# Performance work log

Hardware: AMD Instinct MI355X
Metric: run time of the kernel (lower is better)

## Reference

```python
import jax, jax.numpy as jnp
import numpy as np

D_MODEL = 512
N_HEADS = 8
D_HEAD = D_MODEL // N_HEADS
SCALE = D_HEAD ** -0.5


def _rel_shift(x):
    # x: (b, h, qlen, klen) -> Transformer-XL relative shift
    b, h, qlen, klen = x.shape
    x = jnp.pad(x, ((0, 0), (0, 0), (0, 0), (1, 0)))        # (b,h,q,k+1)
    x = x.reshape(b, h, klen + 1, qlen)
    x = x[:, :, 1:, :].reshape(b, h, qlen, klen)
    return x


def setup_inputs() -> dict:
    key = jax.random.key(0)
    ks = jax.random.split(key, 12)
    B, S = 2, 2048
    P = 2 * S - 1
    w = lambda k, shape: (jax.random.normal(k, shape, jnp.float32) * 0.02)
    return {
        "x": jax.random.normal(ks[0], (B, S, D_MODEL), jnp.float32),
        "pos_emb": jax.random.normal(ks[1], (P, D_MODEL), jnp.float32),
        "Wq": w(ks[2], (D_MODEL, D_MODEL)), "bq": jnp.zeros((D_MODEL,), jnp.float32),
        "Wk": w(ks[3], (D_MODEL, D_MODEL)), "bk": jnp.zeros((D_MODEL,), jnp.float32),
        "Wv": w(ks[4], (D_MODEL, D_MODEL)), "bv": jnp.zeros((D_MODEL,), jnp.float32),
        "Wp": w(ks[5], (D_MODEL, D_MODEL)),
        "Wo": w(ks[6], (D_MODEL, D_MODEL)), "bo": jnp.zeros((D_MODEL,), jnp.float32),
        "pos_bias_u": w(ks[7], (N_HEADS, D_HEAD)),
        "pos_bias_v": w(ks[8], (N_HEADS, D_HEAD)),
    }


def reference(x, pos_emb, Wq, bq, Wk, bk, Wv, bv, Wp, Wo, bo, pos_bias_u, pos_bias_v):
    B, S, _ = x.shape
    # projections (torch Linear: y = x @ W^T + b; here W stored as (in, out))
    q = (x @ Wq + bq).reshape(B, S, N_HEADS, D_HEAD)
    k = (x @ Wk + bk).reshape(B, S, N_HEADS, D_HEAD)
    v = (x @ Wv + bv).reshape(B, S, N_HEADS, D_HEAD)
    p = (pos_emb @ Wp).reshape(-1, N_HEADS, D_HEAD)  # (2S-1, H, D)

    # content score: (q + u) @ k^T  -> (B,H,S,S)
    content = jnp.einsum("bshd,bthd->bhst", q + pos_bias_u, k)
    # position score: (q + v_bias) @ p^T -> (B,H,S,2S-1), then rel_shift
    pos = jnp.einsum("bshd,phd->bhsp", q + pos_bias_v, p)
    pos = _rel_shift(pos)[..., :S]  # trim to kv_len

    attn = jax.nn.softmax((content + pos) * SCALE, axis=-1)
    out = jnp.einsum("bhst,bthd->bshd", attn, v).reshape(B, S, D_MODEL)
    out = out @ Wo + bo
    return out
```

## Files before the change

kernel.cpp:

```cpp
#include <hip/hip_runtime.h>

#define DM    512
#define NH    8
#define DH    64
#define SEQ   2048
#define PLEN  4095
#define NB    2
#define ATT_SCALE 0.125f

typedef __attribute__((ext_vector_type(8))) _Float16 half8;
typedef __attribute__((ext_vector_type(4))) float   floatx4;

__device__ __forceinline__ void gll16(const _Float16* g, _Float16* l) {
    __builtin_amdgcn_global_load_lds(
        (const __attribute__((address_space(1))) void*)g,
        (__attribute__((address_space(3))) void*)l, 16, 0, 0);
}

__global__ __launch_bounds__(256)
void prep(const float* __restrict__ x, const float* __restrict__ pe,
          const float* __restrict__ W0, const float* __restrict__ W1,
          const float* __restrict__ W2, const float* __restrict__ W3,
          const float* __restrict__ W4,
          _Float16* __restrict__ x16, _Float16* __restrict__ pe16,
          _Float16* __restrict__ Wt)
{
    __shared__ _Float16 tile[64 * 72];
    const int z = blockIdx.z;
    const int t = threadIdx.x;

    if (z < 2) {
        const float* src = z ? pe : x;
        _Float16* dst = z ? pe16 : x16;
        const long n = z ? (long)PLEN * DM : (long)NB * SEQ * DM;
        const long i = ((long)blockIdx.x * 256 + t) * 8;
        if (i >= n) return;
        float4 f0 = *(const float4*)(src + i);
        float4 f1 = *(const float4*)(src + i + 4);
        half8 o;
        o[0] = (_Float16)f0.x; o[1] = (_Float16)f0.y;
        o[2] = (_Float16)f0.z; o[3] = (_Float16)f0.w;
        o[4] = (_Float16)f1.x; o[5] = (_Float16)f1.y;
        o[6] = (_Float16)f1.z; o[7] = (_Float16)f1.w;
        *(half8*)(dst + i) = o;
        return;
    }
    if (blockIdx.x >= 64) return;
    const int wz = z - 2;
    const float* W = (wz == 0) ? W0 : (wz == 1) ? W1 : (wz == 2) ? W2
                   : (wz == 3) ? W3 : W4;
    _Float16* dst_base = Wt + (size_t)wz * DM * DM;
    const int n0 = (blockIdx.x & 7) * 64, k0 = (blockIdx.x >> 3) * 64;
    {
        const int kr = t >> 2, nch = (t & 3) * 16;
        const float* src = W + (size_t)(k0 + kr) * DM + n0 + nch;
        float4 f0 = *(const float4*)(src + 0);
        float4 f1 = *(const float4*)(src + 4);
        float4 f2 = *(const float4*)(src + 8);
        float4 f3 = *(const float4*)(src + 12);
        _Float16* trow = &tile[kr * 72 + nch];
        trow[0]  = (_Float16)f0.x; trow[1]  = (_Float16)f0.y;
        trow[2]  = (_Float16)f0.z; trow[3]  = (_Float16)f0.w;
        trow[4]  = (_Float16)f1.x; trow[5]  = (_Float16)f1.y;
        trow[6]  = (_Float16)f1.z; trow[7]  = (_Float16)f1.w;
        trow[8]  = (_Float16)f2.x; trow[9]  = (_Float16)f2.y;
        trow[10] = (_Float16)f2.z; trow[11] = (_Float16)f2.w;
        trow[12] = (_Float16)f3.x; trow[13] = (_Float16)f3.y;
        trow[14] = (_Float16)f3.z; trow[15] = (_Float16)f3.w;
    }
    __syncthreads();
    {
        const int nr = t >> 2, kch = (t & 3) * 16;
        half8 o0, o1;
#pragma unroll
        for (int i = 0; i < 8; ++i) o0[i] = tile[(kch + i) * 72 + nr];
#pragma unroll
        for (int i = 0; i < 8; ++i) o1[i] = tile[(kch + 8 + i) * 72 + nr];
        _Float16* dst = dst_base + (size_t)(n0 + nr) * DM + k0 + kch;
        *(half8*)dst = o0;
        *(half8*)(dst + 8) = o1;
    }
}

__global__ __launch_bounds__(256)
void gemm_qkvp(const _Float16* __restrict__ X, const _Float16* __restrict__ Pe,
               const _Float16* __restrict__ Wt,
               const float* __restrict__ bq, const float* __restrict__ bk,
               const float* __restrict__ bv, const float* __restrict__ bu,
               const float* __restrict__ bvb,
               _Float16* __restrict__ qu16, _Float16* __restrict__ qv16,
               _Float16* __restrict__ k16, _Float16* __restrict__ vt16,
               _Float16* __restrict__ p16)
{
    __shared__ _Float16 smem[32768];

    const int t = threadIdx.x;
    const int w = t >> 6, lane = t & 63, quad = lane >> 4, l16 = lane & 15;
    const int wr = w >> 1, wc = w & 1;
    const int l3 = lane >> 3, pos = lane & 7;
    const int z = blockIdx.z;
    const int n0 = blockIdx.x * 128;
    const int m0 = blockIdx.y * 128;

    const _Float16* A = (z == 3) ? Pe : X;
    const _Float16* Wz = Wt + (size_t)z * DM * DM;

    const int kx = l16 & 7;
    const int hox0 = ((quad) ^ kx) * 8;
    const int hox1 = ((4 + quad) ^ kx) * 8;

    floatx4 acc[4][4];
#pragma unroll
    for (int i = 0; i < 4; ++i)
#pragma unroll
        for (int j = 0; j < 4; ++j) acc[i][j] = (floatx4){0.f, 0.f, 0.f, 0.f};

#define QSTAGE(CUR, K0)                                                        \
    { _Float16* aB = smem + (CUR) * 16384;                                     \
      _Float16* wB = aB + 8192;                                                \
      _Pragma("unroll") for (int I = 0; I < 4; ++I) {                          \
        const int gr = I * 32 + w * 8 + l3;                                    \
        const int ch = pos ^ l3;                                               \
        int ar = m0 + gr; if (z == 3 && ar > PLEN - 1) ar = PLEN - 1;          \
        gll16(A + (size_t)ar * DM + (K0) + ch * 8, aB + I * 2048 + w * 512);   \
        gll16(Wz + (size_t)(n0 + gr) * DM + (K0) + ch * 8,                     \
              wB + I * 2048 + w * 512); } }

    QSTAGE(0, 0);
    int cur = 0;
    for (int k0 = 0; k0 < DM; k0 += 64) {
        asm volatile("s_waitcnt vmcnt(0)" ::: "memory");
        __builtin_amdgcn_s_barrier();
        asm volatile("" ::: "memory");
        if (k0 + 64 < DM) QSTAGE(cur ^ 1, k0 + 64);
        const _Float16* aB = smem + cur * 16384;
        const _Float16* wB = aB + 8192;
#pragma unroll
        for (int kb = 0; kb < 2; ++kb) {
            const int hox = kb ? hox1 : hox0;
            half8 af[4], bf[4];
#pragma unroll
            for (int i = 0; i < 4; ++i)
                af[i] = *(const half8*)&aB[(wr * 64 + i * 16 + l16) * 64 + hox];
#pragma unroll
            for (int j = 0; j < 4; ++j)
                bf[j] = *(const half8*)&wB[(wc * 64 + j * 16 + l16) * 64 + hox];
#pragma unroll
            for (int i = 0; i < 4; ++i)
#pragma unroll
                for (int j = 0; j < 4; ++j)
                    acc[i][j] = __builtin_amdgcn_mfma_f32_16x16x32_f16(
                        af[i], bf[j], acc[i][j], 0, 0, 0);
        }
        cur ^= 1;
    }
#undef QSTAGE

    const int hh = (n0 >> 6) + wc;
    const int bb = m0 >> 11;
    const int sbase = (m0 & 2047) + wr * 64;

    if (z == 0) {
#pragma unroll
        for (int j = 0; j < 4; ++j) {
            const int n = n0 + wc * 64 + j * 16 + l16;
            const int d = j * 16 + l16 - (wc ? 64 : 0) + (wc ? 64 : 0);
            const float bval = bq[n], uval = bu[n], vval = bvb[n];
#pragma unroll
            for (int i = 0; i < 4; ++i)
#pragma unroll
                for (int r = 0; r < 4; ++r) {
                    const int s = sbase + i * 16 + 4 * quad + r;
                    const size_t dst = ((size_t)((hh * NB + bb) * SEQ) + s) * DH + (n & 63);
                    const float q = acc[i][j][r] + bval;
                    qu16[dst] = (_Float16)((q + uval) * ATT_SCALE);
                    qv16[dst] = (_Float16)((q + vval) * ATT_SCALE);
                }
            (void)d;
        }
    } else if (z == 1) {
#pragma unroll
        for (int j = 0; j < 4; ++j) {
            const int n = n0 + wc * 64 + j * 16 + l16;
            const float bval = bk[n];
#pragma unroll
            for (int i = 0; i < 4; ++i)
#pragma unroll
                for (int r = 0; r < 4; ++r) {
                    const int s = sbase + i * 16 + 4 * quad + r;
                    k16[((size_t)((hh * NB + bb) * SEQ) + s) * DH + (n & 63)] =
                        (_Float16)(acc[i][j][r] + bval);
                }
        }
    } else if (z == 2) {
        __syncthreads();
        _Float16* tr = smem;
#pragma unroll
        for (int j = 0; j < 4; ++j) {
            const int ncol = wc * 64 + j * 16 + l16;
            const float bval = bv[n0 + ncol];
#pragma unroll
            for (int i = 0; i < 4; ++i)
#pragma unroll
                for (int r = 0; r < 4; ++r)
                    tr[(wr * 64 + i * 16 + 4 * quad + r) * 132 + ncol] =
                        (_Float16)(acc[i][j][r] + bval);
        }
        __syncthreads();
        {
            const int col = t >> 1;
            const int half = t & 1;
            const int h2 = (n0 + col) >> 6, d = (n0 + col) & 63;
            const int s0 = (m0 & 2047) + half * 64;
            _Float16* dst = vt16 + ((size_t)((h2 * NB + bb) * DH) + d) * SEQ + s0;
#pragma unroll
            for (int c = 0; c < 8; ++c) {
                half8 o;
#pragma unroll
                for (int k = 0; k < 8; ++k)
                    o[k] = tr[(half * 64 + c * 8 + k) * 132 + col];
                *(half8*)(dst + c * 8) = o;
            }
        }
    } else {
#pragma unroll
        for (int j = 0; j < 4; ++j) {
            const int n = n0 + wc * 64 + j * 16 + l16;
#pragma unroll
            for (int i = 0; i < 4; ++i)
#pragma unroll
                for (int r = 0; r < 4; ++r) {
                    const int m = m0 + wr * 64 + i * 16 + 4 * quad + r;
                    if (m < PLEN)
                        p16[((size_t)hh * PLEN + m) * DH + (n & 63)] =
                            (_Float16)acc[i][j][r];
                }
        }
    }
}

__global__ __launch_bounds__(256, 3)
void relattn_mfma(const _Float16* __restrict__ QU,
                  const _Float16* __restrict__ QV,
                  const _Float16* __restrict__ Kp,
                  const _Float16* __restrict__ VT,
                  const _Float16* __restrict__ Pp,
                  float* __restrict__ Opart,
                  float* __restrict__ Lpart)
{
    __shared__ _Float16 kbuf[2 * 4096];
    __shared__ _Float16 vbuf[4096];
    __shared__ _Float16 pring[2 * 4096];
    __shared__ _Float16 tS[64 * 72];

    const int t = threadIdx.x;
    const int w = t >> 6, lane = t & 63, quad = lane >> 4, l16 = lane & 15;
    const int i0 = blockIdx.x * 64;
    const int h = blockIdx.y;
    const int b = blockIdx.z & 1, jh = blockIdx.z >> 1;
    const size_t hb = (size_t)(h * NB + b);
    const int cbase = 48 - 16 * w;
    const int jbeg = jh * (SEQ / 2), jend = jbeg + (SEQ / 2);

    half8 qa[2], va[2];
    {
        const _Float16* qrow = QU + (hb * SEQ + i0 + 16 * w + l16) * DH + quad * 8;
        const _Float16* vrow = QV + (hb * SEQ + i0 + 16 * w + l16) * DH + quad * 8;
        qa[0] = *(const half8*)qrow;       qa[1] = *(const half8*)(qrow + 32);
        va[0] = *(const half8*)vrow;       va[1] = *(const half8*)(vrow + 32);
    }

    floatx4 O[4];
    float lsum[4] = {0.f, 0.f, 0.f, 0.f};
#pragma unroll
    for (int ct = 0; ct < 4; ++ct) O[ct] = (floatx4){0.f, 0.f, 0.f, 0.f};

    const _Float16* Kbase = Kp + hb * SEQ * DH;
    const _Float16* Vbase = VT + hb * DH * SEQ;
    const _Float16* Pbase = Pp + (size_t)h * PLEN * DH;
    const int rbase0 = (SEQ - 1) - i0 - 63;
    const int w0beg  = rbase0 + jbeg;

    const int kx = l16 & 7;
    const int hox0 = ((quad) ^ kx) * 8;
    const int hox1 = ((4 + quad) ^ kx) * 8;

    const int l3 = lane >> 3, pos = lane & 7;

    int prow64[5], pcar[5];
#pragma unroll
    for (int c2 = 0; c2 < 5; ++c2) {
        const int off = cbase + 16 * c2 + l16;
        prow64[c2] = (off & 63) * 64;
        pcar[c2]   = (off >> 6) & 1;
    }

#define STAGE_K(DST, J0)                                                       \
    { _Pragma("unroll") for (int I = 0; I < 2; ++I) {                          \
        const int cid = w * 2 + I;                                             \
        const int row = cid * 8 + l3;                                          \
        gll16(Kbase + (size_t)((J0) + row) * DH + ((pos ^ l3) << 3),           \
              (DST) + cid * 512); } }

#define STAGE_V(J0)                                                            \
    { _Pragma("unroll") for (int I = 0; I < 2; ++I) {                          \
        const int cid = w * 2 + I;                                             \
        const int row = cid * 8 + l3;                                          \
        gll16(Vbase + (size_t)row * SEQ + (J0) + ((pos ^ l3) << 3),            \
              vbuf + cid * 512); } }

#define STAGE_P(RELB)                                                         \
    { _Float16* pdst = pring + ((((RELB) >> 6) & 1) * 4096);                  \
      _Pragma("unroll") for (int I = 0; I < 2; ++I) {                         \
        const int cid = w * 2 + I;                                            \
        int ar = w0beg + (RELB) + cid * 8 + l3;                               \
        if (ar > PLEN - 1) ar = PLEN - 1;                                     \
        gll16(Pbase + (size_t)ar * DH + ((pos ^ l3) << 3),                    \
              pdst + cid * 512); } }

    STAGE_K(kbuf, jbeg);
    STAGE_P(0);
    STAGE_P(64);

    int cur = 0, par = 0;
    for (int j0 = jbeg; j0 < jend; j0 += 64) {
        asm volatile("s_waitcnt vmcnt(0)" ::: "memory");
        __builtin_amdgcn_s_barrier();
        asm volatile("" ::: "memory");

        const _Float16* kS = kbuf + cur * 4096;
        const bool more = (j0 + 64 < jend);

        STAGE_V(j0);
        if (more) STAGE_K(kbuf + (cur ^ 1) * 4096, j0 + 64);

        floatx4 Tacc[5];
#pragma unroll
        for (int c2 = 0; c2 < 5; ++c2) Tacc[c2] = (floatx4){0.f, 0.f, 0.f, 0.f};
#pragma unroll
        for (int c2 = 0; c2 < 5; ++c2) {
            const _Float16* pp = pring + ((pcar[c2] ^ par) * 4096) + prow64[c2];
            half8 bf0 = *(const half8*)(pp + hox0);
            half8 bf1 = *(const half8*)(pp + hox1);
            Tacc[c2] = __builtin_amdgcn_mfma_f32_16x16x32_f16(va[0], bf0, Tacc[c2], 0, 0, 0);
            Tacc[c2] = __builtin_amdgcn_mfma_f32_16x16x32_f16(va[1], bf1, Tacc[c2], 0, 0, 0);
        }

        asm volatile("" ::: "memory");
        __builtin_amdgcn_s_barrier();
        asm volatile("" ::: "memory");
        if (more) STAGE_P((j0 - jbeg) + 128);

        floatx4 Sc[4];
#pragma unroll
        for (int ct = 0; ct < 4; ++ct) Sc[ct] = (floatx4){0.f, 0.f, 0.f, 0.f};
#pragma unroll
        for (int ct = 0; ct < 4; ++ct) {
            half8 bf0 = *(const half8*)&kS[(16 * ct + l16) * 64 + hox0];
            half8 bf1 = *(const half8*)&kS[(16 * ct + l16) * 64 + hox1];
            Sc[ct] = __builtin_amdgcn_mfma_f32_16x16x32_f16(qa[0], bf0, Sc[ct], 0, 0, 0);
            Sc[ct] = __builtin_amdgcn_mfma_f32_16x16x32_f16(qa[1], bf1, Sc[ct], 0, 0, 0);
        }

#pragma unroll
        for (int r = 0; r < 4; ++r) {
            const int u  = l16 - 4 * quad - r + 15;
            const int dl = u & 15;
            const int s  = u >> 4;
            const int pidx = (((quad << 4) | dl) << 2);
            float rot[5];
#pragma unroll
            for (int c2 = 0; c2 < 5; ++c2)
                rot[c2] = __int_as_float(__builtin_amdgcn_ds_bpermute(
                    pidx, __float_as_int(Tacc[c2][r])));
#pragma unroll
            for (int ct = 0; ct < 4; ++ct) {
                const float tv = s ? rot[ct + 1] : rot[ct];
                const float e = __expf(Sc[ct][r] + tv);
                Sc[ct][r] = e;
                lsum[r] += e;
            }
        }

#pragma unroll
        for (int ct = 0; ct < 4; ++ct)
#pragma unroll
            for (int r = 0; r < 4; ++r)
                tS[(16 * w + 4 * quad + r) * 72 + 16 * ct + l16] = (_Float16)Sc[ct][r];
        asm volatile("" ::: "memory");

        if (more) asm volatile("s_waitcnt vmcnt(4)" ::: "memory");
        else      asm volatile("s_waitcnt vmcnt(0)" ::: "memory");
        __builtin_amdgcn_s_barrier();
        asm volatile("" ::: "memory");

#pragma unroll
        for (int kb = 0; kb < 2; ++kb) {
            half8 af = *(const half8*)&tS[(16 * w + l16) * 72 + kb * 32 + quad * 8];
            const int hox = kb ? hox1 : hox0;
#pragma unroll
            for (int ct = 0; ct < 4; ++ct) {
                half8 bf = *(const half8*)&vbuf[(16 * ct + l16) * 64 + hox];
                O[ct] = __builtin_amdgcn_mfma_f32_16x16x32_f16(af, bf, O[ct], 0, 0, 0);
            }
        }
        asm volatile("" ::: "memory");
        cur ^= 1; par ^= 1;
    }
#undef STAGE_K
#undef STAGE_V
#undef STAGE_P

    float* Op = Opart + (size_t)jh * NB * SEQ * DM;
    float* Lp = Lpart + (size_t)jh * NH * NB * SEQ;
#pragma unroll
    for (int r = 0; r < 4; ++r) {
#pragma unroll
        for (int m = 1; m < 16; m <<= 1) lsum[r] += __shfl_xor(lsum[r], m);
        const int row = i0 + 16 * w + 4 * quad + r;
        if (l16 == 0) Lp[hb * SEQ + row] = lsum[r];
        float* orow = Op + (size_t)(b * SEQ + row) * DM + h * DH;
#pragma unroll
        for (int ct = 0; ct < 4; ++ct)
            orow[16 * ct + l16] = O[ct][r];
    }
}

__global__ __launch_bounds__(256)
void attn_combine(const float* __restrict__ O0, const float* __restrict__ O1,
                  const float* __restrict__ L0, const float* __restrict__ L1,
                  _Float16* __restrict__ Out)
{
    const int e = (blockIdx.x * 256 + threadIdx.x) * 8;
    const int m = e >> 9;
    const int col = e & 511;
    const int h = col >> 6;
    const int b = m >> 11, i = m & 2047;
    const int li = (h * NB + b) * SEQ + i;
    const float inv = 1.f / (L0[li] + L1[li]);
    float4 a0 = *(const float4*)(O0 + e);
    float4 a1 = *(const float4*)(O0 + e + 4);
    float4 c0 = *(const float4*)(O1 + e);
    float4 c1 = *(const float4*)(O1 + e + 4);
    half8 o;
    o[0] = (_Float16)((a0.x + c0.x) * inv);
    o[1] = (_Float16)((a0.y + c0.y) * inv);
    o[2] = (_Float16)((a0.z + c0.z) * inv);
    o[3] = (_Float16)((a0.w + c0.w) * inv);
    o[4] = (_Float16)((a1.x + c1.x) * inv);
    o[5] = (_Float16)((a1.y + c1.y) * inv);
    o[6] = (_Float16)((a1.z + c1.z) * inv);
    o[7] = (_Float16)((a1.w + c1.w) * inv);
    *(half8*)(Out + e) = o;
}

__global__ __launch_bounds__(256)
void gemm_out(const _Float16* __restrict__ A, const _Float16* __restrict__ Wt,
              const float* __restrict__ bias, float* __restrict__ Out)
{
    __shared__ _Float16 aS[64 * 72];
    __shared__ _Float16 wS[64 * 72];

    const int t = threadIdx.x;
    const int w = t >> 6, lane = t & 63, quad = lane >> 4, l16 = lane & 15;
    const int n0 = blockIdx.x * 64;
    const int m0 = blockIdx.y * 64;
    const int srow = t >> 2, sch = (t & 3) * 16;

    const _Float16* arowp = A + (size_t)(m0 + srow) * DM + sch;
    const _Float16* wrowp = Wt + (size_t)(n0 + srow) * DM + sch;

    floatx4 acc[4];
#pragma unroll
    for (int ct = 0; ct < 4; ++ct) acc[ct] = (floatx4){0.f, 0.f, 0.f, 0.f};

    half8 pa0 = *(const half8*)arowp;
    half8 pa1 = *(const half8*)(arowp + 8);
    half8 pw0 = *(const half8*)wrowp;
    half8 pw1 = *(const half8*)(wrowp + 8);

    for (int k0 = 0; k0 < DM; k0 += 64) {
        __syncthreads();
        *(half8*)&aS[srow * 72 + sch]     = pa0;
        *(half8*)&aS[srow * 72 + sch + 8] = pa1;
        *(half8*)&wS[srow * 72 + sch]     = pw0;
        *(half8*)&wS[srow * 72 + sch + 8] = pw1;
        __syncthreads();
        if (k0 + 64 < DM) {
            pa0 = *(const half8*)(arowp + k0 + 64);
            pa1 = *(const half8*)(arowp + k0 + 72);
            pw0 = *(const half8*)(wrowp + k0 + 64);
            pw1 = *(const half8*)(wrowp + k0 + 72);
        }
#pragma unroll
        for (int kb = 0; kb < 2; ++kb) {
            half8 af = *(const half8*)&aS[(16 * w + l16) * 72 + kb * 32 + quad * 8];
#pragma unroll
            for (int ct = 0; ct < 4; ++ct) {
                half8 bf = *(const half8*)&wS[(16 * ct + l16) * 72 + kb * 32 + quad * 8];
                acc[ct] = __builtin_amdgcn_mfma_f32_16x16x32_f16(af, bf, acc[ct], 0, 0, 0);
            }
        }
    }

#pragma unroll
    for (int ct = 0; ct < 4; ++ct) {
        const int n = n0 + 16 * ct + l16;
        const float bval = bias[n];
#pragma unroll
        for (int r = 0; r < 4; ++r) {
            const int m = m0 + 16 * w + 4 * quad + r;
            Out[(size_t)m * DM + n] = acc[ct][r] + bval;
        }
    }
}

extern "C" void kernel_launch(void* const* d_in, const int* in_sizes, int n_in,
                              void* d_out, int out_size, void* d_ws, size_t ws_size,
                              hipStream_t stream)
{
    (void)in_sizes; (void)n_in; (void)out_size; (void)ws_size;
    const float* x   = (const float*)d_in[0];
    const float* pe  = (const float*)d_in[1];
    const float* Wq  = (const float*)d_in[2];
    const float* bq  = (const float*)d_in[3];
    const float* Wk  = (const float*)d_in[4];
    const float* bk  = (const float*)d_in[5];
    const float* Wv  = (const float*)d_in[6];
    const float* bv  = (const float*)d_in[7];
    const float* Wp  = (const float*)d_in[8];
    const float* Wo  = (const float*)d_in[9];
    const float* bo  = (const float*)d_in[10];
    const float* pbu = (const float*)d_in[11];
    const float* pbv = (const float*)d_in[12];
    float* out = (float*)d_out;

    const size_t nX  = (size_t)NB * SEQ * DM;
    const size_t nPe = (size_t)PLEN * DM;
    const size_t nW  = (size_t)DM * DM;
    const size_t nH  = (size_t)NH * NB * SEQ * DH;
    const size_t nPh = (size_t)NH * PLEN * DH;
    const size_t nL  = (size_t)NH * NB * SEQ;

    _Float16* x16  = (_Float16*)d_ws;
    _Float16* pe16 = x16 + nX;
    _Float16* wt   = pe16 + nPe;
    _Float16* qu16 = wt + 5 * nW;
    _Float16* qv16 = qu16 + nH;
    _Float16* k16  = qv16 + nH;
    _Float16* vt16 = k16 + nH;
    _Float16* p16  = vt16 + nH;
    _Float16* ow16 = p16 + nPh;
    float*    opart = (float*)(ow16 + nX);
    float*    lpart = opart + 2 * nX;

    dim3 blk(256);
    prep<<<dim3(1024, 1, 7), blk, 0, stream>>>(x, pe, Wq, Wk, Wv, Wp, Wo,
                                               x16, pe16, wt);
    gemm_qkvp<<<dim3(4, 32, 4), blk, 0, stream>>>(x16, pe16, wt,
                                                  bq, bk, bv, pbu, pbv,
                                                  qu16, qv16, k16, vt16, p16);
    relattn_mfma<<<dim3(SEQ / 64, NH, NB * 2), blk, 0, stream>>>(
        qu16, qv16, k16, vt16, p16, opart, lpart);
    attn_combine<<<dim3((unsigned)(nX / (256 * 8))), blk, 0, stream>>>(
        opart, opart + nX, lpart, lpart + nL, ow16);
    gemm_out<<<dim3(8, 64), blk, 0, stream>>>(ow16, wt + 4 * nW, bo, out);
}
```

Measured before the change: 178.3 us.

## Rework attention K/P staging pipeline and retile output GEMM to 128x128 with async LDS loads

In the attention kernel, K is now single-buffered and loaded at the top of each step, while the positional-embedding ring grows to three slots so the next P tile is prefetched before the position MFMAs instead of after them. The waitcnt thresholds are adjusted so the K tile is awaited only before the content-score MFMAs. Separately, the output projection GEMM moves from 64x64 tiles with register-staged loads to 128x128 tiles using double-buffered global_load_lds with swizzled layout and 4x4 MFMA blocking per wave. The new schedule overlaps more P loading with compute, but K latency is now exposed within each step. The larger GEMM tile cuts the grid to 128 blocks and uses 64KB of LDS, which may reduce occupancy.

```diff
diff --git a/kernel.cpp b/kernel.cpp
--- a/kernel.cpp
+++ b/kernel.cpp
@@ -164,7 +164,6 @@
 #pragma unroll
         for (int j = 0; j < 4; ++j) {
             const int n = n0 + wc * 64 + j * 16 + l16;
-            const int d = j * 16 + l16 - (wc ? 64 : 0) + (wc ? 64 : 0);
             const float bval = bq[n], uval = bu[n], vval = bvb[n];
 #pragma unroll
             for (int i = 0; i < 4; ++i)
@@ -176,7 +175,6 @@
                     qu16[dst] = (_Float16)((q + uval) * ATT_SCALE);
                     qv16[dst] = (_Float16)((q + vval) * ATT_SCALE);
                 }
-            (void)d;
         }
     } else if (z == 1) {
 #pragma unroll
@@ -248,9 +246,9 @@
                   float* __restrict__ Opart,
                   float* __restrict__ Lpart)
 {
-    __shared__ _Float16 kbuf[2 * 4096];
+    __shared__ _Float16 kbuf[4096];
     __shared__ _Float16 vbuf[4096];
-    __shared__ _Float16 pring[2 * 4096];
+    __shared__ _Float16 pring[3 * 4096];
     __shared__ _Float16 tS[64 * 72];
 
     const int t = threadIdx.x;
@@ -295,12 +293,12 @@
         pcar[c2]   = (off >> 6) & 1;
     }
 
-#define STAGE_K(DST, J0)                                                       \
+#define STAGE_K(J0)                                                            \
     { _Pragma("unroll") for (int I = 0; I < 2; ++I) {                          \
         const int cid = w * 2 + I;                                             \
         const int row = cid * 8 + l3;                                          \
         gll16(Kbase + (size_t)((J0) + row) * DH + ((pos ^ l3) << 3),           \
-              (DST) + cid * 512); } }
+              kbuf + cid * 512); } }
 
 #define STAGE_V(J0)                                                            \
     { _Pragma("unroll") for (int I = 0; I < 2; ++I) {                          \
@@ -309,55 +307,56 @@
         gll16(Vbase + (size_t)row * SEQ + (J0) + ((pos ^ l3) << 3),            \
               vbuf + cid * 512); } }
 
-#define STAGE_P(RELB)                                                         \
-    { _Float16* pdst = pring + ((((RELB) >> 6) & 1) * 4096);                  \
-      _Pragma("unroll") for (int I = 0; I < 2; ++I) {                         \
-        const int cid = w * 2 + I;                                            \
-        int ar = w0beg + (RELB) + cid * 8 + l3;                               \
-        if (ar > PLEN - 1) ar = PLEN - 1;                                     \
-        gll16(Pbase + (size_t)ar * DH + ((pos ^ l3) << 3),                    \
+#define STAGE_P(RELB, SLOT)                                                    \
+    { _Float16* pdst = pring + (SLOT) * 4096;                                  \
+      _Pragma("unroll") for (int I = 0; I < 2; ++I) {                          \
+        const int cid = w * 2 + I;                                             \
+        int ar = w0beg + (RELB) + cid * 8 + l3;                                \
+        if (ar > PLEN - 1) ar = PLEN - 1;                                      \
+        gll16(Pbase + (size_t)ar * DH + ((pos ^ l3) << 3),                     \
               pdst + cid * 512); } }
 
-    STAGE_K(kbuf, jbeg);
-    STAGE_P(0);
-    STAGE_P(64);
-
-    int cur = 0, par = 0;
+    STAGE_P(0, 0);
+    STAGE_P(64, 1);
+
+    int s_lo = 0, s_hi = 1, s_nx = 2;
     for (int j0 = jbeg; j0 < jend; j0 += 64) {
         asm volatile("s_waitcnt vmcnt(0)" ::: "memory");
         __builtin_amdgcn_s_barrier();
         asm volatile("" ::: "memory");
 
-        const _Float16* kS = kbuf + cur * 4096;
         const bool more = (j0 + 64 < jend);
 
+        STAGE_K(j0);
         STAGE_V(j0);
-        if (more) STAGE_K(kbuf + (cur ^ 1) * 4096, j0 + 64);
-
+        if (more) STAGE_P((j0 - jbeg) + 128, s_nx);
+
+        const _Float16* p_lo = pring + s_lo * 4096;
+        const _Float16* p_hi = pring + s_hi * 4096;
         floatx4 Tacc[5];
 #pragma unroll
         for (int c2 = 0; c2 < 5; ++c2) Tacc[c2] = (floatx4){0.f, 0.f, 0.f, 0.f};
 #pragma unroll
         for (int c2 = 0; c2 < 5; ++c2) {
-            const _Float16* pp = pring + ((pcar[c2] ^ par) * 4096) + prow64[c2];
+            const _Float16* pp = (pcar[c2] ? p_hi : p_lo) + prow64[c2];
             half8 bf0 = *(const half8*)(pp + hox0);
             half8 bf1 = *(const half8*)(pp + hox1);
             Tacc[c2] = __builtin_amdgcn_mfma_f32_16x16x32_f16(va[0], bf0, Tacc[c2], 0, 0, 0);
             Tacc[c2] = __builtin_amdgcn_mfma_f32_16x16x32_f16(va[1], bf1, Tacc[c2], 0, 0, 0);
         }
 
-        asm volatile("" ::: "memory");
+        if (more) asm volatile("s_waitcnt vmcnt(4)" ::: "memory");
+        else      asm volatile("s_waitcnt vmcnt(2)" ::: "memory");
         __builtin_amdgcn_s_barrier();
         asm volatile("" ::: "memory");
-        if (more) STAGE_P((j0 - jbeg) + 128);
 
         floatx4 Sc[4];
 #pragma unroll
         for (int ct = 0; ct < 4; ++ct) Sc[ct] = (floatx4){0.f, 0.f, 0.f, 0.f};
 #pragma unroll
         for (int ct = 0; ct < 4; ++ct) {
-            half8 bf0 = *(const half8*)&kS[(16 * ct + l16) * 64 + hox0];
-            half8 bf1 = *(const half8*)&kS[(16 * ct + l16) * 64 + hox1];
+            half8 bf0 = *(const half8*)&kbuf[(16 * ct + l16) * 64 + hox0];
+            half8 bf1 = *(const half8*)&kbuf[(16 * ct + l16) * 64 + hox1];
             Sc[ct] = __builtin_amdgcn_mfma_f32_16x16x32_f16(qa[0], bf0, Sc[ct], 0, 0, 0);
             Sc[ct] = __builtin_amdgcn_mfma_f32_16x16x32_f16(qa[1], bf1, Sc[ct], 0, 0, 0);
         }
@@ -389,7 +388,7 @@
                 tS[(16 * w + 4 * quad + r) * 72 + 16 * ct + l16] = (_Float16)Sc[ct][r];
         asm volatile("" ::: "memory");
 
-        if (more) asm volatile("s_waitcnt vmcnt(4)" ::: "memory");
+        if (more) asm volatile("s_waitcnt vmcnt(2)" ::: "memory");
         else      asm volatile("s_waitcnt vmcnt(0)" ::: "memory");
         __builtin_amdgcn_s_barrier();
         asm volatile("" ::: "memory");
@@ -405,7 +404,8 @@
             }
         }
         asm volatile("" ::: "memory");
-        cur ^= 1; par ^= 1;
+
+        const int tmp = s_lo; s_lo = s_hi; s_hi = s_nx; s_nx = tmp;
     }
 #undef STAGE_K
 #undef STAGE_V
@@ -458,60 +458,77 @@
 void gemm_out(const _Float16* __restrict__ A, const _Float16* __restrict__ Wt,
               const float* __restrict__ bias, float* __restrict__ Out)
 {
-    __shared__ _Float16 aS[64 * 72];
-    __shared__ _Float16 wS[64 * 72];
+    __shared__ _Float16 smem[32768];
 
     const int t = threadIdx.x;
     const int w = t >> 6, lane = t & 63, quad = lane >> 4, l16 = lane & 15;
-    const int n0 = blockIdx.x * 64;
-    const int m0 = blockIdx.y * 64;
-    const int srow = t >> 2, sch = (t & 3) * 16;
-
-    const _Float16* arowp = A + (size_t)(m0 + srow) * DM + sch;
-    const _Float16* wrowp = Wt + (size_t)(n0 + srow) * DM + sch;
-
-    floatx4 acc[4];
-#pragma unroll
-    for (int ct = 0; ct < 4; ++ct) acc[ct] = (floatx4){0.f, 0.f, 0.f, 0.f};
-
-    half8 pa0 = *(const half8*)arowp;
-    half8 pa1 = *(const half8*)(arowp + 8);
-    half8 pw0 = *(const half8*)wrowp;
-    half8 pw1 = *(const half8*)(wrowp + 8);
-
+    const int wr = w >> 1, wc = w & 1;
+    const int l3 = lane >> 3, pos = lane & 7;
+    const int n0 = blockIdx.x * 128;
+    const int m0 = blockIdx.y * 128;
+
+    const int kx = l16 & 7;
+    const int hox0 = ((quad) ^ kx) * 8;
+    const int hox1 = ((4 + quad) ^ kx) * 8;
+
+    floatx4 acc[4][4];
+#pragma unroll
+    for (int i = 0; i < 4; ++i)
+#pragma unroll
+        for (int j = 0; j < 4; ++j) acc[i][j] = (floatx4){0.f, 0.f, 0.f, 0.f};
+
+#define OSTAGE(CUR, K0)                                                        \
+    { _Float16* aB = smem + (CUR) * 16384;                                     \
+      _Float16* wB = aB + 8192;                                                \
+      _Pragma("unroll") for (int I = 0; I < 4; ++I) {                          \
+        const int gr = I * 32 + w * 8 + l3;                                    \
+        const int ch = pos ^ l3;                                               \
+        gll16(A + (size_t)(m0 + gr) * DM + (K0) + ch * 8,                      \
+              aB + I * 2048 + w * 512);                                        \
+        gll16(Wt + (size_t)(n0 + gr) * DM + (K0) + ch * 8,                     \
+              wB + I * 2048 + w * 512); } }
+
+    OSTAGE(0, 0);
+    int cur = 0;
     for (int k0 = 0; k0 < DM; k0 += 64) {
-        __syncthreads();
-        *(half8*)&aS[srow * 72 + sch]     = pa0;
-        *(half8*)&aS[srow * 72 + sch + 8] = pa1;
-        *(half8*)&wS[srow * 72 + sch]     = pw0;
-        *(half8*)&wS[srow * 72 + sch + 8] = pw1;
-        __syncthreads();
-        if (k0 + 64 < DM) {
-            pa0 = *(const half8*)(arowp + k0 + 64);
-            pa1 = *(const half8*)(arowp + k0 + 72);
-            pw0 = *(const half8*)(wrowp + k0 + 64);
-            pw1 = *(const half8*)(wrowp + k0 + 72);
-        }
+        asm volatile("s_waitcnt vmcnt(0)" ::: "memory");
+        __builtin_amdgcn_s_barrier();
+        asm volatile("" ::: "memory");
+        if (k0 + 64 < DM) OSTAGE(cur ^ 1, k0 + 64);
+        const _Float16* aB = smem + cur * 16384;
+        const _Float16* wB = aB + 8192;
 #pragma unroll
         for (int kb = 0; kb < 2; ++kb) {
-            half8 af = *(const half8*)&aS[(16 * w + l16) * 72 + kb * 32 + quad * 8];
-#pragma unroll
-            for (int ct = 0; ct < 4; ++ct) {
-                half8 bf = *(const half8*)&wS[(16 * ct + l16) * 72 + kb * 32 + quad * 8];
-                acc[ct] = __builtin_amdgcn_mfma_f32_16x16x32_f16(af, bf, acc[ct], 0, 0, 0);
+            const int hox = kb ? hox1 : hox0;
+            half8 af[4], bf[4];
+#pragma unroll
+            for (int i = 0; i < 4; ++i)
+                af[i] = *(const half8*)&aB[(wr * 64 + i * 16 + l16) * 64 + hox];
+#pragma unroll
+            for (int j = 0; j < 4; ++j)
+                bf[j] = *(const half8*)&wB[(wc * 64 + j * 16 + l16) * 64 + hox];
+#pragma unroll
+            for (int i = 0; i < 4; ++i)
+#pragma unroll
+                for (int j = 0; j < 4; ++j)
+                    acc[i][j] = __builtin_amdgcn_mfma_f32_16x16x32_f16(
+                        af[i], bf[j], acc[i][j], 0, 0, 0);
+        }
+        cur ^= 1;
+    }
+#undef OSTAGE
+
+#pragma unroll
+    for (int j = 0; j < 4; ++j) {
+        const int n = n0 + wc * 64 + j * 16 + l16;
+        const float bval = bias[n];
+#pragma unroll
+        for (int i = 0; i < 4; ++i)
+#pragma unroll
+            for (int r = 0; r < 4; ++r) {
+                const int m = m0 + wr * 64 + i * 16 + 4 * quad + r;
+                Out[(size_t)m * DM + n] = acc[i][j][r] + bval;
             }
-        }
-    }
-
-#pragma unroll
-    for (int ct = 0; ct < 4; ++ct) {
-        const int n = n0 + 16 * ct + l16;
-        const float bval = bias[n];
-#pragma unroll
-        for (int r = 0; r < 4; ++r) {
-            const int m = m0 + 16 * w + 4 * quad + r;
-            Out[(size_t)m * DM + n] = acc[ct][r] + bval;
-        }
     }
 }
 
@@ -564,5 +581,5 @@
         qu16, qv16, k16, vt16, p16, opart, lpart);
     attn_combine<<<dim3((unsigned)(nX / (256 * 8))), blk, 0, stream>>>(
         opart, opart + nX, lpart, lpart + nL, ow16);
-    gemm_out<<<dim3(8, 64), blk, 0, stream>>>(ow16, wt + 4 * nW, bo, out);
-}
+    gemm_out<<<dim3(4, 32), blk, 0, stream>>>(ow16, wt + 4 * nW, bo, out);
+}
```

Result: slower. 186.9 us (+4.8%).
